# Kernel tuning notes

Measured on AMD Instinct MI355X. Metric: run time of the kernel, lower is better.

Reference implementation:

```python
import jax, jax.numpy as jnp
import numpy as np

EPS = 1e-8


def setup_inputs() -> dict:
    key = jax.random.key(0)
    k1, k2, k3, k4 = jax.random.split(key, 4)
    N, D, P, H = 8192, 512, 128, 128
    x1 = jax.random.normal(k1, (N, D), dtype=jnp.float32)
    proj_w1 = jax.random.normal(k2, (D, D), dtype=jnp.float32) * (1.0 / np.sqrt(D))
    proj_w2 = jax.random.normal(k3, (D, P), dtype=jnp.float32) * (1.0 / np.sqrt(D))
    gc_w = jax.random.normal(k4, (D, H), dtype=jnp.float32) * (1.0 / np.sqrt(D))
    gc_b = jnp.zeros((H,), dtype=jnp.float32)
    return {"x1": x1, "proj_w1": proj_w1, "proj_w2": proj_w2, "gc_w": gc_w, "gc_b": gc_b}


def _cosine_similarity(x):
    # torch.mm(x, x.T) / clamp(||x|| * ||x||.T, eps)
    w = jnp.sqrt(jnp.sum(x * x, axis=1, keepdims=True))  # [N,1]
    return (x @ x.T) / jnp.maximum(w * w.T, EPS)


def reference(x1, proj_w1, proj_w2, gc_w, gc_b):
    # projector: Linear(512,512,bias=False) -> ReLU -> Linear(512,P,bias=False)
    x_proj = jax.nn.relu(x1 @ proj_w1) @ proj_w2  # [N,P]
    # graph build is under @torch.no_grad(): dense fully-connected weighted graph
    A = jax.lax.stop_gradient(_cosine_similarity(x_proj))  # [N,N]
    N = x1.shape[0]
    # WGraphConv (DGL GraphConv w/ edge weights, norm='both'):
    # fully connected graph incl. self loops -> in_degree = N, norm = N^{-1/2} on both sides
    inv_n = jnp.asarray(1.0 / N, dtype=x1.dtype)
    h = x1 @ gc_w            # project first (D > H, cheaper)  [N,H]
    h = (A @ h) * inv_n      # weighted aggregate, symmetric degree norm
    return h + gc_b          # [N,H]
```

## Files before the change

### kernel.cpp

```cpp
#include <hip/hip_runtime.h>
#include <stdint.h>
#include <stddef.h>

typedef short s16x4 __attribute__((ext_vector_type(4)));
typedef short s16x8 __attribute__((ext_vector_type(8)));
typedef float f32x4 __attribute__((ext_vector_type(4)));

#define NN 8192
#define DD 512
#define PP 128
#define HH 128

__device__ __forceinline__ short f2bf(float f) {
  unsigned u = __builtin_bit_cast(unsigned, f);
  u = (u + 0x7fffu + ((u >> 16) & 1u)) >> 16;
  return (short)u;
}

__device__ __forceinline__ void async16(const void* g, void* l) {
  __builtin_amdgcn_global_load_lds(
      (const __attribute__((address_space(1))) unsigned int*)g,
      (__attribute__((address_space(3))) unsigned int*)l, 16, 0, 0);
}

template <int MF>
__device__ __forceinline__ void gemm_core2(
    const short* __restrict__ A, long lda,
    const short* __restrict__ BT, long ldb,
    long rowBase, long colBase, int k0, int k1,
    short* As0, short* Bs0, short* As1, short* Bs1,
    f32x4 (*acc)[4]) {
  const int tid  = threadIdx.x;
  const int lane = tid & 63;
  const int wid  = tid >> 6;
  const int wr   = (wid >> 1) * (MF * 16);
  const int wc   = (wid & 1) * 64;
  const int srow = lane >> 3;
  const int skk  = (lane & 7) * 8;

#define STAGE_(AS, BS, KK)                                                    \
  do {                                                                        \
    _Pragma("unroll")                                                         \
    for (int it = 0; it < MF; ++it) {                                         \
      int r = wid * (MF * 8) + it * 8;                                        \
      async16(A + (rowBase + r + srow) * lda + (KK) + skk, (AS) + r * 64);    \
    }                                                                         \
    _Pragma("unroll")                                                         \
    for (int it = 0; it < 4; ++it) {                                          \
      int r = wid * 32 + it * 8;                                              \
      async16(BT + (colBase + r + srow) * ldb + (KK) + skk, (BS) + r * 64);   \
    }                                                                         \
  } while (0)

  STAGE_(As0, Bs0, k0);
  __syncthreads();
  for (int k = k0; k < k1; k += 64) {
    if (k + 64 < k1) STAGE_(As1, Bs1, k + 64);
#pragma unroll
    for (int ks = 0; ks < 64; ks += 32) {
      s16x8 af[MF], bfv[4];
#pragma unroll
      for (int i = 0; i < MF; ++i)
        af[i]  = *(const s16x8*)(As0 + (wr + i * 16 + (lane & 15)) * 64 + ks + (lane >> 4) * 8);
#pragma unroll
      for (int i = 0; i < 4; ++i)
        bfv[i] = *(const s16x8*)(Bs0 + (wc + i * 16 + (lane & 15)) * 64 + ks + (lane >> 4) * 8);
#pragma unroll
      for (int mi = 0; mi < MF; ++mi)
#pragma unroll
        for (int ni = 0; ni < 4; ++ni)
          acc[mi][ni] = __builtin_amdgcn_mfma_f32_16x16x32_bf16(af[mi], bfv[ni], acc[mi][ni], 0, 0, 0);
    }
    __syncthreads();
    short* t0 = As0; As0 = As1; As1 = t0;
    short* t1 = Bs0; Bs0 = Bs1; Bs1 = t1;
  }
#undef STAGE_
}

__device__ __forceinline__ void zero_acc2(f32x4 (*acc)[4], int mf) {
  f32x4 z = {0.f, 0.f, 0.f, 0.f};
  for (int i = 0; i < mf; ++i)
    for (int j = 0; j < 4; ++j) acc[i][j] = z;
}

__global__ __launch_bounds__(256) void k_prep(
    const float* __restrict__ x1, const float* __restrict__ w1,
    const float* __restrict__ w2, const float* __restrict__ gcw,
    short* __restrict__ x1b, short* __restrict__ w1t,
    short* __restrict__ w2t, short* __restrict__ gcwt) {
  long b = blockIdx.x;
  int t = threadIdx.x;
  if (b < 4096) {
    long i = b * 256 + t;
    float4 v = ((const float4*)x1)[i];
    s16x4 o;
    o[0] = f2bf(v.x); o[1] = f2bf(v.y); o[2] = f2bf(v.z); o[3] = f2bf(v.w);
    *(s16x4*)(x1b + i * 4) = o;
  } else if (b < 4096 + 1024) {
    long i = (b - 4096) * 256 + t;
    int n = (int)(i >> 9), k = (int)(i & 511);
    w1t[i] = f2bf(w1[(long)k * DD + n]);
  } else if (b < 4096 + 1024 + 256) {
    long i = (b - 5120) * 256 + t;
    int n = (int)(i >> 9), k = (int)(i & 511);
    w2t[i] = f2bf(w2[(long)k * PP + n]);
  } else {
    long i = (b - 5376) * 256 + t;
    int n = (int)(i >> 9), k = (int)(i & 511);
    gcwt[i] = f2bf(gcw[(long)k * HH + n]);
  }
}

__global__ __launch_bounds__(256) void k_g13(const short* __restrict__ x1b,
                                             const short* __restrict__ w1t,
                                             const short* __restrict__ gcwt,
                                             short* __restrict__ Y,
                                             short* __restrict__ hT) {
  __shared__ __align__(16) char smem[65536];
  short* As0 = (short*)smem;
  short* As1 = (short*)(smem + 16384);
  short* Bs0 = (short*)(smem + 32768);
  short* Bs1 = (short*)(smem + 49152);
  f32x4 acc[4][4];
  zero_acc2(acc, 4);
  const int bx = blockIdx.x;
  const int lane = threadIdx.x & 63, wid = threadIdx.x >> 6;
  const int wr = (wid >> 1) * 64, wc = (wid & 1) * 64;
  if (bx < 256) {
    long rowBase = (long)(bx >> 2) * 128;
    long colBase = (long)(bx & 3) * 128;
    gemm_core2<4>(x1b, DD, w1t, DD, rowBase, colBase, 0, DD, As0, Bs0, As1, Bs1, acc);
#pragma unroll
    for (int mi = 0; mi < 4; ++mi)
#pragma unroll
      for (int ni = 0; ni < 4; ++ni)
#pragma unroll
        for (int r = 0; r < 4; ++r) {
          long m = rowBase + wr + mi * 16 + ((lane >> 4) << 2) + r;
          long n = colBase + wc + ni * 16 + (lane & 15);
          float v = acc[mi][ni][r];
          Y[m * DD + n] = f2bf(v > 0.f ? v : 0.f);
        }
  } else {
    long rowBase = (long)(bx - 256) * 128;
    gemm_core2<4>(x1b, DD, gcwt, DD, rowBase, 0, 0, DD, As0, Bs0, As1, Bs1, acc);
    short (*hs)[136] = (short(*)[136])smem;
#pragma unroll
    for (int mi = 0; mi < 4; ++mi)
#pragma unroll
      for (int ni = 0; ni < 4; ++ni)
#pragma unroll
        for (int r = 0; r < 4; ++r) {
          int m = wr + mi * 16 + ((lane >> 4) << 2) + r;
          int n = wc + ni * 16 + (lane & 15);
          hs[n][m] = f2bf(acc[mi][ni][r]);
        }
    __syncthreads();
    int t = threadIdx.x;
    int h = t >> 1, m0 = (t & 1) * 64;
#pragma unroll
    for (int j0 = 0; j0 < 64; j0 += 8) {
      s16x8 o;
#pragma unroll
      for (int u = 0; u < 8; ++u) o[u] = hs[h][m0 + j0 + u];
      *(s16x8*)(hT + (long)h * NN + rowBase + m0 + j0) = o;
    }
  }
}

__global__ __launch_bounds__(256) void k_g2e(const short* __restrict__ Y,
                                             const short* __restrict__ w2t,
                                             const short* __restrict__ hT,
                                             short* __restrict__ xp,
                                             float* __restrict__ invnw,
                                             float* __restrict__ Gp) {
  __shared__ __align__(16) char smem[50176];
  short* As0 = (short*)smem;
  short* As1 = (short*)(smem + 8192);
  short* Bs0 = (short*)(smem + 16384);
  short* Bs1 = (short*)(smem + 32768);
  f32x4 acc[2][4];
  zero_acc2(acc, 2);
  const long rowBase = (long)blockIdx.x * 64;
  gemm_core2<2>(Y, DD, w2t, DD, rowBase, 0, 0, DD, As0, Bs0, As1, Bs1, acc);
  const int t = threadIdx.x;
  const int lane = t & 63, wid = t >> 6;
  {
    const int wr = (wid >> 1) * 32, wc = (wid & 1) * 64;
    float (*xs)[129] = (float(*)[129])smem;
    float* invw_s = (float*)(smem + 49920);
    short* xpt_s = (short*)(smem + 33536);
#pragma unroll
    for (int mi = 0; mi < 2; ++mi)
#pragma unroll
      for (int ni = 0; ni < 4; ++ni)
#pragma unroll
        for (int r = 0; r < 4; ++r)
          xs[wr + mi * 16 + ((lane >> 4) << 2) + r][wc + ni * 16 + (lane & 15)] = acc[mi][ni][r];
    __syncthreads();
    if (t < 64) {
      float s = 0.f;
#pragma unroll 8
      for (int i = 0; i < 128; ++i) { int c = (t + i) & 127; float v = xs[t][c]; s += v * v; }
      float nr = sqrtf(s);
      invnw[rowBase + t] = 1.f / (8192.f * nr);
      invw_s[t] = 1.f / nr;
    }
    __syncthreads();
#pragma unroll
    for (int i = 0; i < 4; ++i) {
      int seg = i * 256 + t;
      int r = seg >> 4, c0 = (seg & 15) * 8;
      s16x8 o;
#pragma unroll
      for (int u = 0; u < 8; ++u) o[u] = f2bf(xs[r][c0 + u]);
      *(s16x8*)(xp + (long)(rowBase + r) * PP + c0) = o;
    }
    int c = t >> 1, n0 = (t & 1) * 32;
#pragma unroll
    for (int j0 = 0; j0 < 32; j0 += 8) {
      s16x8 o;
#pragma unroll
      for (int u = 0; u < 8; ++u) {
        int n = n0 + j0 + u;
        o[u] = f2bf(xs[n][c] * invw_s[n]);
      }
      *(s16x8*)(xpt_s + c * 64 + n0 + j0) = o;
    }
  }
  __syncthreads();
  {
    short* hts = (short*)smem;
    const int srow = lane >> 3, skk = (lane & 7) * 8;
#pragma unroll
    for (int it = 0; it < 4; ++it) {
      int r = wid * 32 + it * 8;
      async16(hT + (long)(r + srow) * NN + rowBase + skk, hts + r * 64);
    }
  }
  __syncthreads();
  {
    const short* xpt_s = (const short*)(smem + 33536);
    const short* hts = (const short*)smem;
    const int wr = (wid >> 1) * 64, wc = (wid & 1) * 64;
    f32x4 acc2[4][4];
    zero_acc2(acc2, 4);
#pragma unroll
    for (int ks = 0; ks < 64; ks += 32) {
      s16x8 af[4], bfv[4];
#pragma unroll
      for (int i = 0; i < 4; ++i)
        af[i]  = *(const s16x8*)(xpt_s + (wr + i * 16 + (lane & 15)) * 64 + ks + (lane >> 4) * 8);
#pragma unroll
      for (int i = 0; i < 4; ++i)
        bfv[i] = *(const s16x8*)(hts + (wc + i * 16 + (lane & 15)) * 64 + ks + (lane >> 4) * 8);
#pragma unroll
      for (int mi = 0; mi < 4; ++mi)
#pragma unroll
        for (int ni = 0; ni < 4; ++ni)
          acc2[mi][ni] = __builtin_amdgcn_mfma_f32_16x16x32_bf16(af[mi], bfv[ni], acc2[mi][ni], 0, 0, 0);
    }
    float* gp = Gp + (long)blockIdx.x * (PP * HH);
#pragma unroll
    for (int mi = 0; mi < 4; ++mi)
#pragma unroll
      for (int ni = 0; ni < 4; ++ni)
#pragma unroll
        for (int r = 0; r < 4; ++r) {
          int m = wr + mi * 16 + ((lane >> 4) << 2) + r;
          int n = wc + ni * 16 + (lane & 15);
          gp[m * HH + n] = acc2[mi][ni][r];
        }
  }
}

__global__ __launch_bounds__(256) void k_red(const float* __restrict__ Gp,
                                             short* __restrict__ GT) {
  int i = blockIdx.x * 256 + threadIdx.x;
  float s = 0.f;
#pragma unroll 8
  for (int j = 0; j < 128; ++j) s += Gp[j * (PP * HH) + i];
  int p = i >> 7, h = i & 127;
  GT[h * PP + p] = f2bf(s);
}

__global__ __launch_bounds__(256) void k_gf(const short* __restrict__ xp,
                                            const short* __restrict__ GT,
                                            const float* __restrict__ invnw,
                                            const float* __restrict__ gcb,
                                            float* __restrict__ out) {
  __shared__ __align__(16) char smem[49152];
  short* As0 = (short*)smem;
  short* As1 = (short*)(smem + 8192);
  short* Bs0 = (short*)(smem + 16384);
  short* Bs1 = (short*)(smem + 32768);
  f32x4 acc[2][4];
  zero_acc2(acc, 2);
  long rowBase = (long)blockIdx.x * 64;
  gemm_core2<2>(xp, PP, GT, PP, rowBase, 0, 0, PP, As0, Bs0, As1, Bs1, acc);
  const int lane = threadIdx.x & 63, wid = threadIdx.x >> 6;
  const int wr = (wid >> 1) * 32, wc = (wid & 1) * 64;
#pragma unroll
  for (int mi = 0; mi < 2; ++mi)
#pragma unroll
    for (int ni = 0; ni < 4; ++ni)
#pragma unroll
      for (int r = 0; r < 4; ++r) {
        long m = rowBase + wr + mi * 16 + ((lane >> 4) << 2) + r;
        int n = wc + ni * 16 + (lane & 15);
        out[m * HH + n] = acc[mi][ni][r] * invnw[m] + gcb[n];
      }
}

extern "C" void kernel_launch(void* const* d_in, const int* in_sizes, int n_in,
                              void* d_out, int out_size, void* d_ws, size_t ws_size,
                              hipStream_t stream) {
  const float* x1  = (const float*)d_in[0];
  const float* w1  = (const float*)d_in[1];
  const float* w2  = (const float*)d_in[2];
  const float* gcw = (const float*)d_in[3];
  const float* gcb = (const float*)d_in[4];
  float* out = (float*)d_out;

  char* ws = (char*)d_ws;
  size_t off = 0;
  auto alloc = [&](size_t bytes) -> char* {
    char* p = ws + off;
    off += (bytes + 255) & ~(size_t)255;
    return p;
  };
  short* x1b  = (short*)alloc((size_t)NN * DD * 2);
  short* w1t  = (short*)alloc((size_t)DD * DD * 2);
  short* w2t  = (short*)alloc((size_t)PP * DD * 2);
  short* gcwt = (short*)alloc((size_t)HH * DD * 2);
  short* Y    = (short*)alloc((size_t)NN * DD * 2);
  short* xp   = (short*)alloc((size_t)NN * PP * 2);
  short* hT   = (short*)alloc((size_t)NN * HH * 2);
  float* invnw = (float*)alloc((size_t)NN * 4);
  float* Gp   = (float*)alloc((size_t)128 * PP * HH * 4);
  short* GT   = (short*)alloc((size_t)PP * HH * 2);

  hipLaunchKernelGGL(k_prep, dim3(5632), dim3(256), 0, stream,
                     x1, w1, w2, gcw, x1b, w1t, w2t, gcwt);
  hipLaunchKernelGGL(k_g13, dim3(320), dim3(256), 0, stream, x1b, w1t, gcwt, Y, hT);
  hipLaunchKernelGGL(k_g2e, dim3(128), dim3(256), 0, stream, Y, w2t, hT, xp, invnw, Gp);
  hipLaunchKernelGGL(k_red, dim3(64), dim3(256), 0, stream, Gp, GT);
  hipLaunchKernelGGL(k_gf, dim3(128), dim3(256), 0, stream, xp, GT, invnw, gcb, out);
}
```

Baseline: 54.42 us.

## Split k_g13 into smaller 64x128 tiles with two-wave blocks for more parallelism

The fused GEMM1/GEMM3 kernel now uses 64-row tiles with 128-thread blocks (two waves, each covering 64 columns) and launches 640 blocks instead of 320, using an inlined double-buffered async-LDS pipeline in place of the shared gemm_core2 helper. The goal is to fill the 256 CUs of the GPU better, since 320 blocks leaves many CUs with uneven load. In exchange each block reuses its A tile less, and each wave now loads all four A fragments, which adds global and LDS traffic per FLOP. The LDS footprint shrinks to 48 KB, which may let more blocks reside on each CU.

```diff
diff --git a/kernel.cpp b/kernel.cpp
--- a/kernel.cpp
+++ b/kernel.cpp
@@ -112,59 +112,98 @@
   }
 }
 
-__global__ __launch_bounds__(256) void k_g13(const short* __restrict__ x1b,
+__global__ __launch_bounds__(128) void k_g13(const short* __restrict__ x1b,
                                              const short* __restrict__ w1t,
                                              const short* __restrict__ gcwt,
                                              short* __restrict__ Y,
                                              short* __restrict__ hT) {
-  __shared__ __align__(16) char smem[65536];
+  __shared__ __align__(16) char smem[49152];
   short* As0 = (short*)smem;
-  short* As1 = (short*)(smem + 16384);
-  short* Bs0 = (short*)(smem + 32768);
-  short* Bs1 = (short*)(smem + 49152);
+  short* As1 = (short*)(smem + 8192);
+  short* Bs0 = (short*)(smem + 16384);
+  short* Bs1 = (short*)(smem + 32768);
   f32x4 acc[4][4];
   zero_acc2(acc, 4);
+  const int tid = threadIdx.x;
+  const int lane = tid & 63, wid = tid >> 6;
+  const int srow = lane >> 3, skk = (lane & 7) * 8;
   const int bx = blockIdx.x;
-  const int lane = threadIdx.x & 63, wid = threadIdx.x >> 6;
-  const int wr = (wid >> 1) * 64, wc = (wid & 1) * 64;
-  if (bx < 256) {
-    long rowBase = (long)(bx >> 2) * 128;
-    long colBase = (long)(bx & 3) * 128;
-    gemm_core2<4>(x1b, DD, w1t, DD, rowBase, colBase, 0, DD, As0, Bs0, As1, Bs1, acc);
+  const bool isG1 = bx < 512;
+  const long rowBase = isG1 ? (long)(bx >> 2) * 64 : (long)(bx - 512) * 64;
+  const long colBase = isG1 ? (long)(bx & 3) * 128 : 0;
+  const short* BT = isG1 ? w1t : gcwt;
+
+#define STAGE_(AS, BS, KK)                                                    \
+  do {                                                                        \
+    _Pragma("unroll")                                                         \
+    for (int it = 0; it < 4; ++it) {                                          \
+      int r = wid * 32 + it * 8;                                              \
+      async16(x1b + (rowBase + r + srow) * DD + (KK) + skk, (AS) + r * 64);   \
+    }                                                                         \
+    _Pragma("unroll")                                                         \
+    for (int it = 0; it < 8; ++it) {                                          \
+      int r = wid * 64 + it * 8;                                              \
+      async16(BT + (colBase + r + srow) * DD + (KK) + skk, (BS) + r * 64);    \
+    }                                                                         \
+  } while (0)
+
+  STAGE_(As0, Bs0, 0);
+  __syncthreads();
+  for (int k = 0; k < DD; k += 64) {
+    if (k + 64 < DD) STAGE_(As1, Bs1, k + 64);
+#pragma unroll
+    for (int ks = 0; ks < 64; ks += 32) {
+      s16x8 af[4], bfv[4];
+#pragma unroll
+      for (int i = 0; i < 4; ++i)
+        af[i]  = *(const s16x8*)(As0 + (i * 16 + (lane & 15)) * 64 + ks + (lane >> 4) * 8);
+#pragma unroll
+      for (int i = 0; i < 4; ++i)
+        bfv[i] = *(const s16x8*)(Bs0 + (wid * 64 + i * 16 + (lane & 15)) * 64 + ks + (lane >> 4) * 8);
+#pragma unroll
+      for (int mi = 0; mi < 4; ++mi)
+#pragma unroll
+        for (int ni = 0; ni < 4; ++ni)
+          acc[mi][ni] = __builtin_amdgcn_mfma_f32_16x16x32_bf16(af[mi], bfv[ni], acc[mi][ni], 0, 0, 0);
+    }
+    __syncthreads();
+    short* t0 = As0; As0 = As1; As1 = t0;
+    short* t1 = Bs0; Bs0 = Bs1; Bs1 = t1;
+  }
+#undef STAGE_
+
+  if (isG1) {
 #pragma unroll
     for (int mi = 0; mi < 4; ++mi)
 #pragma unroll
       for (int ni = 0; ni < 4; ++ni)
 #pragma unroll
         for (int r = 0; r < 4; ++r) {
-          long m = rowBase + wr + mi * 16 + ((lane >> 4) << 2) + r;
-          long n = colBase + wc + ni * 16 + (lane & 15);
+          long m = rowBase + mi * 16 + ((lane >> 4) << 2) + r;
+          long n = colBase + wid * 64 + ni * 16 + (lane & 15);
           float v = acc[mi][ni][r];
           Y[m * DD + n] = f2bf(v > 0.f ? v : 0.f);
         }
   } else {
-    long rowBase = (long)(bx - 256) * 128;
-    gemm_core2<4>(x1b, DD, gcwt, DD, rowBase, 0, 0, DD, As0, Bs0, As1, Bs1, acc);
-    short (*hs)[136] = (short(*)[136])smem;
+    short (*hs)[66] = (short(*)[66])smem;
 #pragma unroll
     for (int mi = 0; mi < 4; ++mi)
 #pragma unroll
       for (int ni = 0; ni < 4; ++ni)
 #pragma unroll
         for (int r = 0; r < 4; ++r) {
-          int m = wr + mi * 16 + ((lane >> 4) << 2) + r;
-          int n = wc + ni * 16 + (lane & 15);
+          int m = mi * 16 + ((lane >> 4) << 2) + r;
+          int n = wid * 64 + ni * 16 + (lane & 15);
           hs[n][m] = f2bf(acc[mi][ni][r]);
         }
     __syncthreads();
-    int t = threadIdx.x;
-    int h = t >> 1, m0 = (t & 1) * 64;
+    int h = tid;
 #pragma unroll
     for (int j0 = 0; j0 < 64; j0 += 8) {
       s16x8 o;
 #pragma unroll
-      for (int u = 0; u < 8; ++u) o[u] = hs[h][m0 + j0 + u];
-      *(s16x8*)(hT + (long)h * NN + rowBase + m0 + j0) = o;
+      for (int u = 0; u < 8; ++u) o[u] = hs[h][j0 + u];
+      *(s16x8*)(hT + (long)h * NN + rowBase + j0) = o;
     }
   }
 }
@@ -343,7 +382,7 @@
 
   hipLaunchKernelGGL(k_prep, dim3(5632), dim3(256), 0, stream,
                      x1, w1, w2, gcw, x1b, w1t, w2t, gcwt);
-  hipLaunchKernelGGL(k_g13, dim3(320), dim3(256), 0, stream, x1b, w1t, gcwt, Y, hT);
+  hipLaunchKernelGGL(k_g13, dim3(640), dim3(128), 0, stream, x1b, w1t, gcwt, Y, hT);
   hipLaunchKernelGGL(k_g2e, dim3(128), dim3(256), 0, stream, Y, w2t, hT, xp, invnw, Gp);
   hipLaunchKernelGGL(k_red, dim3(64), dim3(256), 0, stream, Gp, GT);
   hipLaunchKernelGGL(k_gf, dim3(128), dim3(256), 0, stream, xp, GT, invnw, gcb, out);
```

Result: faster. 50.46 us (-7.3%).
